# Performance work log

Hardware: AMD Instinct MI355X
Metric: run time of the kernel (lower is better)

The kernel has to match this reference:

```python
import jax, jax.numpy as jnp
import numpy as np

DT = 0.005
BETA = 0.9
THR = 0.5
TAU_MIN = 0.02
TAU_STEP = 0.03
TAU_R = 0.002
SLOPE = 25.0  # snntorch fast_sigmoid default surrogate slope

@jax.custom_vjp
def spike_fn(x):
    return (x > 0).astype(x.dtype)

def _spike_fwd(x):
    return spike_fn(x), x

def _spike_bwd(x, g):
    return (g / (SLOPE * jnp.abs(x) + 1.0) ** 2,)

spike_fn.defvjp(_spike_fwd, _spike_bwd)

def setup_inputs() -> dict:
    key = jax.random.key(0)
    ks = jax.random.split(key, 8)
    T, NIN, H, NOUT, P = 1000, 4, 4096, 2, 16
    inv_sqrt_h = 1.0 / np.sqrt(H).astype(np.float32)
    return {
        "x": jax.random.normal(ks[0], (T, NIN + 2, 1), jnp.float32),
        "noise": jax.random.normal(ks[1], (T, H, 1), jnp.float32),
        "Win": jax.random.normal(ks[2], (H, NIN + 2), jnp.float32),
        "Wout": jax.random.normal(ks[3], (NOUT, H), jnp.float32) * inv_sqrt_h,
        "pin": jax.random.normal(ks[4], (H, P), jnp.float32) * inv_sqrt_h,
        "pout": jax.random.normal(ks[5], (H, P), jnp.float32) * inv_sqrt_h,
        "l": jax.random.normal(ks[6], (P,), jnp.float32) * inv_sqrt_h,
        "sigmoid_tau_d": jax.random.normal(ks[7], (H, 1), jnp.float32),
    }

def reference(x, noise, Win, Wout, pin, pout, l, sigmoid_tau_d):
    H = Win.shape[0]
    tau_d = jax.nn.sigmoid(sigmoid_tau_d) * TAU_STEP + TAU_MIN   # [H,1]
    Wr = (l * pin) @ pout.T                                      # [H,H] low-rank recurrent matrix
    decay_r = jnp.exp(jnp.asarray(-DT / TAU_R, x.dtype))         # scalar
    decay_d = jnp.exp(-DT / tau_d)                               # [H,1]
    s_gain = DT / (tau_d * TAU_R)                                # [H,1]

    def step(carry, inp):
        mem, r, s = carry
        xi, ni = inp
        I = Win @ xi + Wr @ r + ni / 10.0                        # [H,1]
        # snntorch Leaky, reset_mechanism='subtract': reset from incoming mem (detached)
        reset = jax.lax.stop_gradient(spike_fn(mem - THR))
        mem = BETA * mem + I - reset * THR
        spk = spike_fn(mem - THR)
        s = s * decay_r + s_gain * spk
        r = decay_d * r + DT * s
        return (mem, r, s), r

    z = jnp.zeros((H, 1), x.dtype)
    _, R = jax.lax.scan(step, (z, z, z), (x, noise))             # R: [T,H,1]
    y = jnp.einsum('oh,thj->toj', Wout, R)                       # [T,O,1]
    return y
```

## Files before the change

### kernel.cpp

```cpp
#include <hip/hip_runtime.h>
#include <math.h>

#define KB       4
#define NTHREADS 512
#define NW       (NTHREADS/64)
#define HID      4096
#define HB       (HID / KB)
#define TT       1000
#define PP       16
#define SLOTW    24

#define BETA 0.9f
#define THRV 0.5f
#define DTV  0.005f

__global__ __launch_bounds__(NTHREADS, 1)
void snn_kernel(const float* __restrict__ x,
                const float* __restrict__ noise,
                const float* __restrict__ Win,
                const float* __restrict__ Wout,
                const float* __restrict__ pin,
                const float* __restrict__ pout,
                const float* __restrict__ lvec,
                const float* __restrict__ stdv,
                float* __restrict__ out,
                unsigned long long* __restrict__ slots)
{
    const int b    = blockIdx.x;
    const int tid  = threadIdx.x;
    const int wave = tid >> 6;
    const int lane = tid & 63;
    const int h0   = b * HB + tid * 2;
    const int h1   = h0 + 1;

    const bool lb0 = (lane & 1) != 0;
    const bool lb1 = (lane & 2) != 0;
    const bool lb2 = (lane & 4) != 0;
    const bool lb3 = (lane & 8) != 0;

    const int rb0 = (b == 0) ? 1 : 0;
    const int rb1 = (b <= 1) ? 2 : 1;
    const int rb2 = (b <= 2) ? 3 : 2;

    __shared__ float part[NW][20];
    __shared__ float ubuf[NW][16];

    float lv[PP];
    #pragma unroll
    for (int p = 0; p < PP; p += 4) {
        float4 t4 = *(const float4*)&lvec[p];
        lv[p] = t4.x; lv[p+1] = t4.y; lv[p+2] = t4.z; lv[p+3] = t4.w;
    }
    float pl0[PP], pl1[PP], po0[PP], po1[PP];
    #pragma unroll
    for (int p = 0; p < PP; p += 4) {
        float4 a = *(const float4*)&pin[h0*PP + p];
        float4 c = *(const float4*)&pin[h1*PP + p];
        pl0[p]   = a.x*lv[p];   pl0[p+1] = a.y*lv[p+1];
        pl0[p+2] = a.z*lv[p+2]; pl0[p+3] = a.w*lv[p+3];
        pl1[p]   = c.x*lv[p];   pl1[p+1] = c.y*lv[p+1];
        pl1[p+2] = c.z*lv[p+2]; pl1[p+3] = c.w*lv[p+3];
        float4 e = *(const float4*)&pout[h0*PP + p];
        float4 f = *(const float4*)&pout[h1*PP + p];
        po0[p]   = e.x; po0[p+1] = e.y; po0[p+2] = e.z; po0[p+3] = e.w;
        po1[p]   = f.x; po1[p+1] = f.y; po1[p+2] = f.z; po1[p+3] = f.w;
    }
    const float2* win2 = (const float2*)Win;
    float2 wa0 = win2[h0*3], wb0 = win2[h0*3+1], wc0 = win2[h0*3+2];
    float2 wa1 = win2[h1*3], wb1 = win2[h1*3+1], wc1 = win2[h1*3+2];
    float2 wo_a = *(const float2*)&Wout[h0];
    float2 wo_b = *(const float2*)&Wout[HID + h0];

    float2 sd = *(const float2*)&stdv[h0];
    float sig0 = 1.f / (1.f + expf(-sd.x));
    float sig1 = 1.f / (1.f + expf(-sd.y));
    float tau0 = sig0 * 0.03f + 0.02f;
    float tau1 = sig1 * 0.03f + 0.02f;
    float dd0  = expf(-DTV / tau0);
    float dd1  = expf(-DTV / tau1);
    float sg0  = DTV / (tau0 * 0.002f);
    float sg1  = DTV / (tau1 * 0.002f);
    const float DECAY_R = expf(-2.5f);

    float mem0 = 0.f, mem1 = 0.f, r0 = 0.f, r1 = 0.f, s0 = 0.f, s1 = 0.f;

    const float2* x2 = (const float2*)x;
    float2 nz = *(const float2*)&noise[h0];
    float2 xa = x2[0], xb = x2[1], xc = x2[2];

    float uu[16];
    #pragma unroll
    for (int p = 0; p < 16; ++p) uu[p] = 0.f;

    for (int t = 0; t <= TT; ++t) {
        float2 nz_n = nz, xa_n = xa, xb_n = xb, xc_n = xc;
        if (t < TT - 1) {
            const int tn = t + 1;
            nz_n = *(const float2*)&noise[tn * HID + h0];
            xa_n = x2[tn*3]; xb_n = x2[tn*3+1]; xc_n = x2[tn*3+2];
        }

        if (t > 0) {
            const int par = t & 1;
            float pa[18];
            #pragma unroll
            for (int p = 0; p < PP; ++p) pa[p] = po0[p]*r0 + po1[p]*r1;
            pa[16] = wo_a.x*r0 + wo_a.y*r1;
            pa[17] = wo_b.x*r0 + wo_b.y*r1;

            float a1[8], yv;
            #pragma unroll
            for (int k = 0; k < 8; ++k) {
                float keep = lb0 ? pa[2*k+1] : pa[2*k];
                float send = lb0 ? pa[2*k]   : pa[2*k+1];
                a1[k] = keep + __shfl_xor(send, 1, 64);
            }
            {
                float keep = lb0 ? pa[17] : pa[16];
                float send = lb0 ? pa[16] : pa[17];
                yv = keep + __shfl_xor(send, 1, 64);
            }
            float a2[4];
            #pragma unroll
            for (int k = 0; k < 4; ++k) {
                float keep = lb1 ? a1[2*k+1] : a1[2*k];
                float send = lb1 ? a1[2*k]   : a1[2*k+1];
                a2[k] = keep + __shfl_xor(send, 2, 64);
            }
            yv += __shfl_xor(yv, 2, 64);
            float a3[2];
            #pragma unroll
            for (int k = 0; k < 2; ++k) {
                float keep = lb2 ? a2[2*k+1] : a2[2*k];
                float send = lb2 ? a2[2*k]   : a2[2*k+1];
                a3[k] = keep + __shfl_xor(send, 4, 64);
            }
            yv += __shfl_xor(yv, 4, 64);
            float uv;
            {
                float keep = lb3 ? a3[1] : a3[0];
                float send = lb3 ? a3[0] : a3[1];
                uv = keep + __shfl_xor(send, 8, 64);
            }
            yv += __shfl_xor(yv, 8, 64);
            uv += __shfl_xor(uv, 16, 64);
            uv += __shfl_xor(uv, 32, 64);
            yv += __shfl_xor(yv, 16, 64);
            yv += __shfl_xor(yv, 32, 64);

            if (lane < 18) part[wave][lane] = (lane < 16) ? uv : yv;
            __syncthreads();

            float bs = 0.f;
            if (lane < 18) {
                float q01 = part[0][lane] + part[1][lane];
                float q23 = part[2][lane] + part[3][lane];
                float q45 = part[4][lane] + part[5][lane];
                float q67 = part[6][lane] + part[7][lane];
                bs = (q01 + q23) + (q45 + q67);
            }

            if (wave == 0 && lane < 18) {
                union { float f; unsigned u; } cv; cv.f = bs;
                unsigned long long pk = ((unsigned long long)(unsigned)t << 32)
                                      | (unsigned long long)cv.u;
                __hip_atomic_store(&slots[(size_t)(par*KB + b)*SLOTW + lane], pk,
                                   __ATOMIC_RELAXED, __HIP_MEMORY_SCOPE_AGENT);
            }

            if (t < TT || b == 0) {
                float f0 = 0.f, f1 = 0.f, f2 = 0.f;
                if (lane < 18) {
                    const unsigned long long* p0 =
                        &slots[(size_t)(par*KB + rb0)*SLOTW + lane];
                    const unsigned long long* p1 =
                        &slots[(size_t)(par*KB + rb1)*SLOTW + lane];
                    const unsigned long long* p2 =
                        &slots[(size_t)(par*KB + rb2)*SLOTW + lane];
                    unsigned long long v0, v1, v2;
                    int spin = 0;
                    do {
                        v0 = __hip_atomic_load(p0, __ATOMIC_RELAXED,
                                               __HIP_MEMORY_SCOPE_AGENT);
                        v1 = __hip_atomic_load(p1, __ATOMIC_RELAXED,
                                               __HIP_MEMORY_SCOPE_AGENT);
                        v2 = __hip_atomic_load(p2, __ATOMIC_RELAXED,
                                               __HIP_MEMORY_SCOPE_AGENT);
                    } while ((((int)(v0 >> 32) != t) | ((int)(v1 >> 32) != t) |
                              ((int)(v2 >> 32) != t)) && ++spin < (1 << 20));
                    union { unsigned u; float f; } c0, c1, c2;
                    c0.u = (unsigned)v0; c1.u = (unsigned)v1; c2.u = (unsigned)v2;
                    f0 = c0.f; f1 = c1.f; f2 = c2.f;
                }
                float total = (b < 2) ? ((bs + f0) + (f1 + f2))
                                      : ((f0 + f1) + (f2 + bs));
                if (lane < 16) ubuf[wave][lane] = total;
                if (b == 0 && wave == 0 && lane >= 16 && lane < 18)
                    out[(t-1)*2 + (lane - 16)] = total;

                float4 u0 = *(const float4*)&ubuf[wave][0];
                float4 u1 = *(const float4*)&ubuf[wave][4];
                float4 u2 = *(const float4*)&ubuf[wave][8];
                float4 u3 = *(const float4*)&ubuf[wave][12];
                uu[0]=u0.x; uu[1]=u0.y; uu[2]=u0.z; uu[3]=u0.w;
                uu[4]=u1.x; uu[5]=u1.y; uu[6]=u1.z; uu[7]=u1.w;
                uu[8]=u2.x; uu[9]=u2.y; uu[10]=u2.z; uu[11]=u2.w;
                uu[12]=u3.x; uu[13]=u3.y; uu[14]=u3.z; uu[15]=u3.w;
            }
        }

        if (t < TT) {
            float rec0 = 0.f, rec1 = 0.f;
            #pragma unroll
            for (int p = 0; p < PP; ++p) { rec0 += pl0[p]*uu[p]; rec1 += pl1[p]*uu[p]; }
            float xw0 = wa0.x*xa.x + wa0.y*xa.y + wb0.x*xb.x + wb0.y*xb.y
                      + wc0.x*xc.x + wc0.y*xc.y;
            float xw1 = wa1.x*xa.x + wa1.y*xa.y + wb1.x*xb.x + wb1.y*xb.y
                      + wc1.x*xc.x + wc1.y*xc.y;
            float I0 = (xw0 + rec0) + nz.x / 10.0f;
            float I1 = (xw1 + rec1) + nz.y / 10.0f;

            float rst0 = (mem0 - THRV > 0.f) ? THRV : 0.f;
            float rst1 = (mem1 - THRV > 0.f) ? THRV : 0.f;
            mem0 = BETA*mem0 + I0 - rst0;
            mem1 = BETA*mem1 + I1 - rst1;
            float spk0 = (mem0 - THRV > 0.f) ? 1.f : 0.f;
            float spk1 = (mem1 - THRV > 0.f) ? 1.f : 0.f;
            s0 = s0*DECAY_R + sg0*spk0;
            s1 = s1*DECAY_R + sg1*spk1;
            r0 = dd0*r0 + DTV*s0;
            r1 = dd1*r1 + DTV*s1;

            nz = nz_n; xa = xa_n; xb = xb_n; xc = xc_n;
        }
    }
}

extern "C" void kernel_launch(void* const* d_in, const int* in_sizes, int n_in,
                              void* d_out, int out_size, void* d_ws, size_t ws_size,
                              hipStream_t stream)
{
    const float* x     = (const float*)d_in[0];
    const float* noise = (const float*)d_in[1];
    const float* Win   = (const float*)d_in[2];
    const float* Wout  = (const float*)d_in[3];
    const float* pin   = (const float*)d_in[4];
    const float* pout  = (const float*)d_in[5];
    const float* l     = (const float*)d_in[6];
    const float* stdv  = (const float*)d_in[7];
    float* out = (float*)d_out;
    unsigned long long* slots = (unsigned long long*)d_ws;

    hipLaunchKernelGGL(snn_kernel, dim3(KB), dim3(NTHREADS), 0, stream,
                       x, noise, Win, Wout, pin, pout, l, stdv,
                       out, slots);
}
```

Measured before the change: 1.679 ms.

## Halve block threads to 4 neurons each and use DPP for intra-row reductions

Each block now has 256 threads (4 waves), and each thread handles 4 hidden units instead of 2. This cuts the cross-wave shared-memory reduction to 4 partials and makes the per-step __syncthreads barrier cheaper. The xor-1/2/8 lane shuffles become DPP row operations (quad_perm and row_ror), which avoids LDS-based permutes. The trade is more serial per-thread work and more registers per step, and the per-step critical path is latency-bound.

```diff
diff --git a/kernel.cpp b/kernel.cpp
--- a/kernel.cpp
+++ b/kernel.cpp
@@ -2,10 +2,11 @@
 #include <math.h>
 
 #define KB       4
-#define NTHREADS 512
-#define NW       (NTHREADS/64)
+#define NTHREADS 256
+#define NW       4
 #define HID      4096
 #define HB       (HID / KB)
+#define NPT      4
 #define TT       1000
 #define PP       16
 #define SLOTW    24
@@ -13,6 +14,12 @@
 #define BETA 0.9f
 #define THRV 0.5f
 #define DTV  0.005f
+
+template<int CTRL>
+__device__ __forceinline__ float dppx(float v) {
+    return __int_as_float(__builtin_amdgcn_update_dpp(
+        0, __float_as_int(v), CTRL, 0xF, 0xF, true));
+}
 
 __global__ __launch_bounds__(NTHREADS, 1)
 void snn_kernel(const float* __restrict__ x,
@@ -30,8 +37,7 @@
     const int tid  = threadIdx.x;
     const int wave = tid >> 6;
     const int lane = tid & 63;
-    const int h0   = b * HB + tid * 2;
-    const int h1   = h0 + 1;
+    const int h0   = b * HB + tid * NPT;
 
     const bool lb0 = (lane & 1) != 0;
     const bool lb1 = (lane & 2) != 0;
@@ -51,41 +57,50 @@
         float4 t4 = *(const float4*)&lvec[p];
         lv[p] = t4.x; lv[p+1] = t4.y; lv[p+2] = t4.z; lv[p+3] = t4.w;
     }
-    float pl0[PP], pl1[PP], po0[PP], po1[PP];
-    #pragma unroll
-    for (int p = 0; p < PP; p += 4) {
-        float4 a = *(const float4*)&pin[h0*PP + p];
-        float4 c = *(const float4*)&pin[h1*PP + p];
-        pl0[p]   = a.x*lv[p];   pl0[p+1] = a.y*lv[p+1];
-        pl0[p+2] = a.z*lv[p+2]; pl0[p+3] = a.w*lv[p+3];
-        pl1[p]   = c.x*lv[p];   pl1[p+1] = c.y*lv[p+1];
-        pl1[p+2] = c.z*lv[p+2]; pl1[p+3] = c.w*lv[p+3];
-        float4 e = *(const float4*)&pout[h0*PP + p];
-        float4 f = *(const float4*)&pout[h1*PP + p];
-        po0[p]   = e.x; po0[p+1] = e.y; po0[p+2] = e.z; po0[p+3] = e.w;
-        po1[p]   = f.x; po1[p+1] = f.y; po1[p+2] = f.z; po1[p+3] = f.w;
-    }
-    const float2* win2 = (const float2*)Win;
-    float2 wa0 = win2[h0*3], wb0 = win2[h0*3+1], wc0 = win2[h0*3+2];
-    float2 wa1 = win2[h1*3], wb1 = win2[h1*3+1], wc1 = win2[h1*3+2];
-    float2 wo_a = *(const float2*)&Wout[h0];
-    float2 wo_b = *(const float2*)&Wout[HID + h0];
-
-    float2 sd = *(const float2*)&stdv[h0];
-    float sig0 = 1.f / (1.f + expf(-sd.x));
-    float sig1 = 1.f / (1.f + expf(-sd.y));
-    float tau0 = sig0 * 0.03f + 0.02f;
-    float tau1 = sig1 * 0.03f + 0.02f;
-    float dd0  = expf(-DTV / tau0);
-    float dd1  = expf(-DTV / tau1);
-    float sg0  = DTV / (tau0 * 0.002f);
-    float sg1  = DTV / (tau1 * 0.002f);
+    float pl[NPT][PP], po[NPT][PP];
+    #pragma unroll
+    for (int j = 0; j < NPT; ++j) {
+        #pragma unroll
+        for (int p = 0; p < PP; p += 4) {
+            float4 a = *(const float4*)&pin[(h0+j)*PP + p];
+            pl[j][p]   = a.x*lv[p];   pl[j][p+1] = a.y*lv[p+1];
+            pl[j][p+2] = a.z*lv[p+2]; pl[j][p+3] = a.w*lv[p+3];
+            float4 e = *(const float4*)&pout[(h0+j)*PP + p];
+            po[j][p]   = e.x; po[j][p+1] = e.y;
+            po[j][p+2] = e.z; po[j][p+3] = e.w;
+        }
+    }
+    float win[NPT][6];
+    #pragma unroll
+    for (int j = 0; j < NPT; ++j) {
+        const float2* wr = (const float2*)&Win[(h0+j)*6];
+        float2 wA = wr[0], wB = wr[1], wC = wr[2];
+        win[j][0]=wA.x; win[j][1]=wA.y; win[j][2]=wB.x;
+        win[j][3]=wB.y; win[j][4]=wC.x; win[j][5]=wC.y;
+    }
+    float4 woa = *(const float4*)&Wout[h0];
+    float4 wob = *(const float4*)&Wout[HID + h0];
+
+    float4 sd4 = *(const float4*)&stdv[h0];
+    float dd[NPT], sg[NPT];
+    {
+        float sdv[4] = { sd4.x, sd4.y, sd4.z, sd4.w };
+        #pragma unroll
+        for (int j = 0; j < NPT; ++j) {
+            float sig = 1.f / (1.f + expf(-sdv[j]));
+            float tau = sig * 0.03f + 0.02f;
+            dd[j] = expf(-DTV / tau);
+            sg[j] = DTV / (tau * 0.002f);
+        }
+    }
     const float DECAY_R = expf(-2.5f);
 
-    float mem0 = 0.f, mem1 = 0.f, r0 = 0.f, r1 = 0.f, s0 = 0.f, s1 = 0.f;
+    float mem[NPT], rr[NPT], ss[NPT];
+    #pragma unroll
+    for (int j = 0; j < NPT; ++j) { mem[j] = 0.f; rr[j] = 0.f; ss[j] = 0.f; }
 
     const float2* x2 = (const float2*)x;
-    float2 nz = *(const float2*)&noise[h0];
+    float4 nz = *(const float4*)&noise[h0];
     float2 xa = x2[0], xb = x2[1], xc = x2[2];
 
     float uu[16];
@@ -93,10 +108,10 @@
     for (int p = 0; p < 16; ++p) uu[p] = 0.f;
 
     for (int t = 0; t <= TT; ++t) {
-        float2 nz_n = nz, xa_n = xa, xb_n = xb, xc_n = xc;
+        float4 nz_n = nz; float2 xa_n = xa, xb_n = xb, xc_n = xc;
         if (t < TT - 1) {
             const int tn = t + 1;
-            nz_n = *(const float2*)&noise[tn * HID + h0];
+            nz_n = *(const float4*)&noise[tn * HID + h0];
             xa_n = x2[tn*3]; xb_n = x2[tn*3+1]; xc_n = x2[tn*3+2];
         }
 
@@ -104,30 +119,32 @@
             const int par = t & 1;
             float pa[18];
             #pragma unroll
-            for (int p = 0; p < PP; ++p) pa[p] = po0[p]*r0 + po1[p]*r1;
-            pa[16] = wo_a.x*r0 + wo_a.y*r1;
-            pa[17] = wo_b.x*r0 + wo_b.y*r1;
+            for (int p = 0; p < PP; ++p)
+                pa[p] = (po[0][p]*rr[0] + po[1][p]*rr[1])
+                      + (po[2][p]*rr[2] + po[3][p]*rr[3]);
+            pa[16] = (woa.x*rr[0] + woa.y*rr[1]) + (woa.z*rr[2] + woa.w*rr[3]);
+            pa[17] = (wob.x*rr[0] + wob.y*rr[1]) + (wob.z*rr[2] + wob.w*rr[3]);
 
             float a1[8], yv;
             #pragma unroll
             for (int k = 0; k < 8; ++k) {
                 float keep = lb0 ? pa[2*k+1] : pa[2*k];
                 float send = lb0 ? pa[2*k]   : pa[2*k+1];
-                a1[k] = keep + __shfl_xor(send, 1, 64);
+                a1[k] = keep + dppx<0xB1>(send);
             }
             {
                 float keep = lb0 ? pa[17] : pa[16];
                 float send = lb0 ? pa[16] : pa[17];
-                yv = keep + __shfl_xor(send, 1, 64);
+                yv = keep + dppx<0xB1>(send);
             }
             float a2[4];
             #pragma unroll
             for (int k = 0; k < 4; ++k) {
                 float keep = lb1 ? a1[2*k+1] : a1[2*k];
                 float send = lb1 ? a1[2*k]   : a1[2*k+1];
-                a2[k] = keep + __shfl_xor(send, 2, 64);
-            }
-            yv += __shfl_xor(yv, 2, 64);
+                a2[k] = keep + dppx<0x4E>(send);
+            }
+            yv += dppx<0x4E>(yv);
             float a3[2];
             #pragma unroll
             for (int k = 0; k < 2; ++k) {
@@ -140,9 +157,9 @@
             {
                 float keep = lb3 ? a3[1] : a3[0];
                 float send = lb3 ? a3[0] : a3[1];
-                uv = keep + __shfl_xor(send, 8, 64);
-            }
-            yv += __shfl_xor(yv, 8, 64);
+                uv = keep + dppx<0x128>(send);
+            }
+            yv += dppx<0x128>(yv);
             uv += __shfl_xor(uv, 16, 64);
             uv += __shfl_xor(uv, 32, 64);
             yv += __shfl_xor(yv, 16, 64);
@@ -153,11 +170,8 @@
 
             float bs = 0.f;
             if (lane < 18) {
-                float q01 = part[0][lane] + part[1][lane];
-                float q23 = part[2][lane] + part[3][lane];
-                float q45 = part[4][lane] + part[5][lane];
-                float q67 = part[6][lane] + part[7][lane];
-                bs = (q01 + q23) + (q45 + q67);
+                bs = (part[0][lane] + part[1][lane])
+                   + (part[2][lane] + part[3][lane]);
             }
 
             if (wave == 0 && lane < 18) {
@@ -210,27 +224,28 @@
         }
 
         if (t < TT) {
-            float rec0 = 0.f, rec1 = 0.f;
-            #pragma unroll
-            for (int p = 0; p < PP; ++p) { rec0 += pl0[p]*uu[p]; rec1 += pl1[p]*uu[p]; }
-            float xw0 = wa0.x*xa.x + wa0.y*xa.y + wb0.x*xb.x + wb0.y*xb.y
-                      + wc0.x*xc.x + wc0.y*xc.y;
-            float xw1 = wa1.x*xa.x + wa1.y*xa.y + wb1.x*xb.x + wb1.y*xb.y
-                      + wc1.x*xc.x + wc1.y*xc.y;
-            float I0 = (xw0 + rec0) + nz.x / 10.0f;
-            float I1 = (xw1 + rec1) + nz.y / 10.0f;
-
-            float rst0 = (mem0 - THRV > 0.f) ? THRV : 0.f;
-            float rst1 = (mem1 - THRV > 0.f) ? THRV : 0.f;
-            mem0 = BETA*mem0 + I0 - rst0;
-            mem1 = BETA*mem1 + I1 - rst1;
-            float spk0 = (mem0 - THRV > 0.f) ? 1.f : 0.f;
-            float spk1 = (mem1 - THRV > 0.f) ? 1.f : 0.f;
-            s0 = s0*DECAY_R + sg0*spk0;
-            s1 = s1*DECAY_R + sg1*spk1;
-            r0 = dd0*r0 + DTV*s0;
-            r1 = dd1*r1 + DTV*s1;
-
+            float nzv[4] = { nz.x, nz.y, nz.z, nz.w };
+            #pragma unroll
+            for (int j = 0; j < NPT; ++j) {
+                float ra = pl[j][0]*uu[0];
+                float rb2_ = pl[j][8]*uu[8];
+                #pragma unroll
+                for (int p = 1; p < 8; ++p) {
+                    ra   += pl[j][p]*uu[p];
+                    rb2_ += pl[j][p+8]*uu[p+8];
+                }
+                float rec = ra + rb2_;
+                float xw = win[j][0]*xa.x + win[j][1]*xa.y
+                         + win[j][2]*xb.x + win[j][3]*xb.y
+                         + win[j][4]*xc.x + win[j][5]*xc.y;
+                float I = (xw + rec) + nzv[j] / 10.0f;
+
+                float rst = (mem[j] - THRV > 0.f) ? THRV : 0.f;
+                mem[j] = BETA*mem[j] + I - rst;
+                float spk = (mem[j] - THRV > 0.f) ? 1.f : 0.f;
+                ss[j] = ss[j]*DECAY_R + sg[j]*spk;
+                rr[j] = dd[j]*rr[j] + DTV*ss[j];
+            }
             nz = nz_n; xa = xa_n; xb = xb_n; xc = xc_n;
         }
     }
```

After: 1.631 ms. 1.03x faster.
